# Kernel tuning notes

Hardware: AMD Instinct MI355X
Metric: run time of the kernel (lower is better)

The kernel has to match this reference:

```python
import jax, jax.numpy as jnp
import numpy as np

# --- constants matching init_kwargs / defaults in the torch module ---
N_HID = 1024
N_INP = 1
DT = 0.05
RHO = 0.99
INPUT_SCALING = 1.0
GAMMA_RANGE = (2.0, 3.0)
EPS_RANGE = (0.5, 1.5)
THETA = 0.1        # spike threshold (default arg of cell)
TAU_MEM = 20.0     # LI filter time constant (default arg of forward_li_features)
FADING = False


def setup_inputs() -> dict:
    key = jax.random.key(0)
    B, T = 128, 500
    x = jax.random.normal(key, (B, T, N_INP), dtype=jnp.float32)

    rng = np.random.default_rng(0)
    # h2h = 2*(2*rand-1), then spectral_norm_scaling to spectral radius rho
    h2h = 2.0 * (2.0 * rng.random((N_HID, N_HID)) - 1.0)
    cur_rho = np.max(np.abs(np.linalg.eigvals(h2h)))
    h2h = (h2h * (RHO / cur_rho)).astype(np.float32)
    x2h = (rng.random((N_INP, N_HID)) * INPUT_SCALING).astype(np.float32)
    bias = ((rng.random(N_HID) * 2.0 - 1.0) * INPUT_SCALING).astype(np.float32)
    gamma = (rng.random(N_HID) * (GAMMA_RANGE[1] - GAMMA_RANGE[0]) + GAMMA_RANGE[0]).astype(np.float32)
    epsilon = (rng.random(N_HID) * (EPS_RANGE[1] - EPS_RANGE[0]) + EPS_RANGE[0]).astype(np.float32)

    return {
        "x": x,
        "h2h": jnp.asarray(h2h),
        "x2h": jnp.asarray(x2h),
        "bias": jnp.asarray(bias),
        "gamma": jnp.asarray(gamma),
        "epsilon": jnp.asarray(epsilon),
    }


def reference(x, h2h, x2h, bias, gamma, epsilon):
    B, T, _ = x.shape
    n_hid = h2h.shape[0]
    dt = jnp.float32(DT)
    alpha = jnp.exp(jnp.float32(-1.0 / TAU_MEM))

    def step(carry, xt):
        hy, hz, u, tot = carry
        # coupled-oscillator cell (ref_period stays identically zero in the source)
        pre = jnp.tanh(xt @ x2h + hy @ h2h + bias)       # (B, n_hid)
        hz = hz + dt * (pre - gamma * hy - epsilon * hz)
        if FADING:
            hz = hz - dt * hz
        hy = hy + dt * hz
        if FADING:
            hy = hy - dt * hy
        s = (hy - THETA > 0).astype(jnp.float32)          # spike
        u = u * alpha + s * (1.0 - alpha)                 # LI filter
        tot = tot + s.sum()
        return (hy, hz, u, tot), None

    z = jnp.zeros((B, n_hid), dtype=jnp.float32)
    init = (z, z, z, jnp.float32(0.0))
    xs = jnp.swapaxes(x, 0, 1)                            # (T, B, n_inp)
    (hy, hz, u, tot), _ = jax.lax.scan(step, init, xs)
    avg_firing_rate = tot / (B * T * n_hid)
    return u, avg_firing_rate
```

## Files before the change

kernel.cpp:

```cpp
#include <hip/hip_runtime.h>
#include <math.h>

#define N_HID   1024
#define NBATCH  128
#define TSTEPS  500
#define DT      0.05f
#define THETA   0.1f

#define B_WG   8
#define C_WG   64
#define KSPL   8
#define KSEG   (N_HID / KSPL)
#define NGRP   (NBATCH / B_WG)
#define NCT    (N_HID / C_WG)
#define NWG    (NGRP * NCT)

typedef unsigned long long u64;


__global__ __launch_bounds__(256, 1) void persist_kernel(
    const float* __restrict__ x,
    const float* __restrict__ W,
    const float* __restrict__ x2h,
    const float* __restrict__ bias,
    const float* __restrict__ gam,
    const float* __restrict__ eps,
    float* __restrict__ hyT0,
    float* __restrict__ hyT1,
    float* __restrict__ uout,
    unsigned int* __restrict__ tot,
    unsigned int* __restrict__ bar,
    float alpha, float oma)
{
    __shared__ float sh_hyT[N_HID * B_WG];
    __shared__ float sh_part[KSPL * B_WG * C_WG];
    __shared__ float sh_out[C_WG * (B_WG + 1)];
    __shared__ unsigned int sh_cnt;

    const int tid = threadIdx.x;
    if (tid == 0) sh_cnt = 0u;

    const int bid   = blockIdx.x;
    const int xcd   = bid & 7;
    const int idx   = bid >> 3;
    const int ctile = xcd * 2 + (idx & 1);
    const int btile = idx >> 1;
    const int c0g   = ctile * C_WG;
    const int b0    = btile * B_WG;

    const int cg  = tid & 15;
    const int bg  = (tid >> 4) & 1;
    const int ks  = tid >> 5;
    const int bl0 = bg * 4;
    const int k0  = ks * KSEG;
    const float* Wp = W + (size_t)k0 * N_HID + c0g + cg * 4;

    const int bl_a = tid >> 6;
    const int bl_b = 4 + bl_a;
    const int c_e  = tid & 63;
    const int cgl  = c0g + c_e;
    const float x2h_c  = x2h[cgl];
    const float bias_c = bias[cgl];
    const float gam_c  = gam[cgl];
    const float eps_c  = eps[cgl];
    const float* xrow_a = x + (size_t)(b0 + bl_a) * TSTEPS;
    const float* xrow_b = x + (size_t)(b0 + bl_b) * TSTEPS;

    float hz_a = 0.f, hz_b = 0.f, u_a = 0.f, u_b = 0.f;
    unsigned int spikes = 0;

    unsigned int* mybar = bar + (btile << 6);

    const float* bufs[2] = { hyT0, hyT1 };

    for (int t = 0; t < TSTEPS; ++t) {
        const float* src = bufs[t & 1];
        float*       dst = (float*)bufs[(t + 1) & 1];

        {
            u64 tmp[16];
            #pragma unroll
            for (int it = 0; it < 16; ++it) {
                const int i    = it * 256 + tid;
                const int k    = i >> 2;
                const int pair = i & 3;
                const u64* sp = (const u64*)(src + (size_t)k * NBATCH + b0) + pair;
                tmp[it] = __hip_atomic_load(sp, __ATOMIC_RELAXED,
                                            __HIP_MEMORY_SCOPE_AGENT);
            }
            u64* s64 = (u64*)sh_hyT;
            #pragma unroll
            for (int it = 0; it < 16; ++it)
                s64[it * 256 + tid] = tmp[it];
        }
        __syncthreads();

        float acc[4][4];
        #pragma unroll
        for (int i = 0; i < 4; ++i)
            #pragma unroll
            for (int j = 0; j < 4; ++j) acc[i][j] = 0.f;

        #pragma unroll 8
        for (int kk = 0; kk < KSEG; ++kk) {
            const float4 hv = *(const float4*)(&sh_hyT[(k0 + kk) * B_WG + bl0]);
            const float4 wv = *(const float4*)(Wp + (size_t)kk * N_HID);
            acc[0][0] = fmaf(hv.x, wv.x, acc[0][0]);
            acc[0][1] = fmaf(hv.x, wv.y, acc[0][1]);
            acc[0][2] = fmaf(hv.x, wv.z, acc[0][2]);
            acc[0][3] = fmaf(hv.x, wv.w, acc[0][3]);
            acc[1][0] = fmaf(hv.y, wv.x, acc[1][0]);
            acc[1][1] = fmaf(hv.y, wv.y, acc[1][1]);
            acc[1][2] = fmaf(hv.y, wv.z, acc[1][2]);
            acc[1][3] = fmaf(hv.y, wv.w, acc[1][3]);
            acc[2][0] = fmaf(hv.z, wv.x, acc[2][0]);
            acc[2][1] = fmaf(hv.z, wv.y, acc[2][1]);
            acc[2][2] = fmaf(hv.z, wv.z, acc[2][2]);
            acc[2][3] = fmaf(hv.z, wv.w, acc[2][3]);
            acc[3][0] = fmaf(hv.w, wv.x, acc[3][0]);
            acc[3][1] = fmaf(hv.w, wv.y, acc[3][1]);
            acc[3][2] = fmaf(hv.w, wv.z, acc[3][2]);
            acc[3][3] = fmaf(hv.w, wv.w, acc[3][3]);
        }

        #pragma unroll
        for (int bi = 0; bi < 4; ++bi) {
            float4 v = make_float4(acc[bi][0], acc[bi][1], acc[bi][2], acc[bi][3]);
            *(float4*)(&sh_part[((ks * B_WG) + bl0 + bi) * C_WG + cg * 4]) = v;
        }
        __syncthreads();

        {
            float sum = sh_part[(0 * B_WG + bl_a) * C_WG + c_e];
            #pragma unroll
            for (int s2 = 1; s2 < KSPL; ++s2)
                sum += sh_part[(s2 * B_WG + bl_a) * C_WG + c_e];
            const float xb  = xrow_a[t];
            const float pre = tanhf(fmaf(xb, x2h_c, sum) + bias_c);
            const float hyv = sh_hyT[cgl * B_WG + bl_a];
            hz_a = fmaf(DT, pre - gam_c * hyv - eps_c * hz_a, hz_a);
            const float hyn = fmaf(DT, hz_a, hyv);
            const int s = ((hyn - THETA) > 0.f) ? 1 : 0;
            u_a = fmaf(u_a, alpha, (float)s * oma);
            spikes += (unsigned)s;
            sh_out[c_e * (B_WG + 1) + bl_a] = hyn;
        }
        {
            float sum = sh_part[(0 * B_WG + bl_b) * C_WG + c_e];
            #pragma unroll
            for (int s2 = 1; s2 < KSPL; ++s2)
                sum += sh_part[(s2 * B_WG + bl_b) * C_WG + c_e];
            const float xb  = xrow_b[t];
            const float pre = tanhf(fmaf(xb, x2h_c, sum) + bias_c);
            const float hyv = sh_hyT[cgl * B_WG + bl_b];
            hz_b = fmaf(DT, pre - gam_c * hyv - eps_c * hz_b, hz_b);
            const float hyn = fmaf(DT, hz_b, hyv);
            const int s = ((hyn - THETA) > 0.f) ? 1 : 0;
            u_b = fmaf(u_b, alpha, (float)s * oma);
            spikes += (unsigned)s;
            sh_out[c_e * (B_WG + 1) + bl_b] = hyn;
        }
        __syncthreads();

        {
            const int c2 = tid >> 2;
            const int b2 = (tid & 3) * 2;
            u64 v;
            float2 f2 = make_float2(sh_out[c2 * (B_WG + 1) + b2],
                                    sh_out[c2 * (B_WG + 1) + b2 + 1]);
            __builtin_memcpy(&v, &f2, 8);
            u64* dp = (u64*)(dst + (size_t)(c0g + c2) * NBATCH + b0 + b2);
            __hip_atomic_store(dp, v, __ATOMIC_RELAXED,
                               __HIP_MEMORY_SCOPE_AGENT);
        }
        __syncthreads();

        if (tid == 0) {
            __hip_atomic_fetch_add(mybar, 1u, __ATOMIC_RELAXED,
                                   __HIP_MEMORY_SCOPE_AGENT);
            const unsigned int target = 16u * (unsigned int)(t + 1);
            while (__hip_atomic_load(mybar, __ATOMIC_RELAXED,
                                     __HIP_MEMORY_SCOPE_AGENT) < target) {
                __builtin_amdgcn_s_sleep(1);
            }
        }
        __syncthreads();
    }

    uout[(size_t)(b0 + bl_a) * N_HID + cgl] = u_a;
    uout[(size_t)(b0 + bl_b) * N_HID + cgl] = u_b;

    unsigned int s = spikes;
    s += __shfl_down(s, 32);
    s += __shfl_down(s, 16);
    s += __shfl_down(s, 8);
    s += __shfl_down(s, 4);
    s += __shfl_down(s, 2);
    s += __shfl_down(s, 1);
    if ((tid & 63) == 0) atomicAdd(&sh_cnt, s);
    __syncthreads();
    if (tid == 0) atomicAdd(tot, sh_cnt);
}

__global__ void init_kernel(float* hyT0, unsigned int* tot, unsigned int* bar)
{
    const int i = blockIdx.x * blockDim.x + threadIdx.x;
    const int n = NBATCH * N_HID;
    if (i < n) hyT0[i] = 0.f;
    if (i == 0) *tot = 0u;
    if (i < NGRP * 64) bar[i] = 0u;
}

__global__ void final_kernel(const unsigned int* __restrict__ tot,
                             float* __restrict__ out_rate)
{
    if (threadIdx.x == 0 && blockIdx.x == 0) {
        const double denom = (double)NBATCH * (double)TSTEPS * (double)N_HID;
        *out_rate = (float)((double)(*tot) / denom);
    }
}

extern "C" void kernel_launch(void* const* d_in, const int* in_sizes, int n_in,
                              void* d_out, int out_size, void* d_ws, size_t ws_size,
                              hipStream_t stream)
{
    const float* x    = (const float*)d_in[0];
    const float* h2h  = (const float*)d_in[1];
    const float* x2h  = (const float*)d_in[2];
    const float* bias = (const float*)d_in[3];
    const float* gam  = (const float*)d_in[4];
    const float* eps  = (const float*)d_in[5];

    float* out = (float*)d_out;

    float* hyT0 = (float*)d_ws;
    float* hyT1 = hyT0 + (size_t)NBATCH * N_HID;
    unsigned int* tot = (unsigned int*)(hyT1 + (size_t)NBATCH * N_HID);
    unsigned int* bar = tot + 64;

    init_kernel<<<dim3((NBATCH * N_HID + 255) / 256), dim3(256), 0, stream>>>(
        hyT0, tot, bar);

    float alpha = expf(-1.0f / 20.0f);
    float oma   = 1.0f - alpha;

    void* args[] = {
        (void*)&x, (void*)&h2h, (void*)&x2h, (void*)&bias, (void*)&gam,
        (void*)&eps, (void*)&hyT0, (void*)&hyT1, (void*)&out, (void*)&tot,
        (void*)&bar, (void*)&alpha, (void*)&oma
    };
    hipLaunchCooperativeKernel((const void*)persist_kernel,
                               dim3(NWG), dim3(256), args, 0, stream);

    final_kernel<<<dim3(1), dim3(64), 0, stream>>>(tot, out + (size_t)NBATCH * N_HID);
}
```

Measured before the change: 3.762 ms.

## Replace group counter barrier with per-tile step flags polled per wave

The shared atomic-counter barrier, where every workgroup increments and spins, is replaced by per-column-tile step flags. Each wave polls only the four flags for the producer tiles whose hidden-state slice it loads, then loads that slice straight into its own shared region. This removes the block-wide sync after the load and one after the barrier, so waves can start their partial GEMV as soon as their inputs are ready. The first step now zero-fills shared memory instead of reading a zeroed global buffer. The gain depends on relaxed-ordering flags correctly publishing data, and one leftover no-op loop remains.

```diff
diff --git a/kernel.cpp b/kernel.cpp
--- a/kernel.cpp
+++ b/kernel.cpp
@@ -1,5 +1,8 @@
 #include <hip/hip_runtime.h>
 #include <math.h>
+
+typedef unsigned long long u64;
+typedef unsigned int u32;
 
 #define N_HID   1024
 #define NBATCH  128
@@ -15,8 +18,22 @@
 #define NCT    (N_HID / C_WG)
 #define NWG    (NGRP * NCT)
 
-typedef unsigned long long u64;
-
+#define CTRL_TOT    0
+#define CTRL_GRP    64
+#define CTRL_WORDS  (CTRL_GRP + NGRP * 64)
+
+__device__ __forceinline__ u32 a_ld32(const u32* p) {
+    return __hip_atomic_load(p, __ATOMIC_RELAXED, __HIP_MEMORY_SCOPE_AGENT);
+}
+__device__ __forceinline__ void a_st32(u32* p, u32 v) {
+    __hip_atomic_store(p, v, __ATOMIC_RELAXED, __HIP_MEMORY_SCOPE_AGENT);
+}
+__device__ __forceinline__ u64 a_ld64(const u64* p) {
+    return __hip_atomic_load(p, __ATOMIC_RELAXED, __HIP_MEMORY_SCOPE_AGENT);
+}
+__device__ __forceinline__ void a_st64(u64* p, u64 v) {
+    __hip_atomic_store(p, v, __ATOMIC_RELAXED, __HIP_MEMORY_SCOPE_AGENT);
+}
 
 __global__ __launch_bounds__(256, 1) void persist_kernel(
     const float* __restrict__ x,
@@ -28,14 +45,13 @@
     float* __restrict__ hyT0,
     float* __restrict__ hyT1,
     float* __restrict__ uout,
-    unsigned int* __restrict__ tot,
-    unsigned int* __restrict__ bar,
+    u32* __restrict__ ctrl,
     float alpha, float oma)
 {
     __shared__ float sh_hyT[N_HID * B_WG];
     __shared__ float sh_part[KSPL * B_WG * C_WG];
     __shared__ float sh_out[C_WG * (B_WG + 1)];
-    __shared__ unsigned int sh_cnt;
+    __shared__ u32 sh_cnt;
 
     const int tid = threadIdx.x;
     if (tid == 0) sh_cnt = 0u;
@@ -54,6 +70,11 @@
     const int bl0 = bg * 4;
     const int k0  = ks * KSEG;
     const float* Wp = W + (size_t)k0 * N_HID + c0g + cg * 4;
+
+    const int wv   = tid >> 6;
+    const int lane = tid & 63;
+    u32* flags = ctrl + CTRL_GRP + (btile << 6);
+    u32* myflag_pollp = flags + (4 * wv + (lane & 3));
 
     const int bl_a = tid >> 6;
     const int bl_b = 4 + bl_a;
@@ -67,60 +88,61 @@
     const float* xrow_b = x + (size_t)(b0 + bl_b) * TSTEPS;
 
     float hz_a = 0.f, hz_b = 0.f, u_a = 0.f, u_b = 0.f;
-    unsigned int spikes = 0;
-
-    unsigned int* mybar = bar + (btile << 6);
-
-    const float* bufs[2] = { hyT0, hyT1 };
+    u32 spikes = 0;
+
+    const float* src = hyT0;
+    float*       dst = hyT1;
 
     for (int t = 0; t < TSTEPS; ++t) {
-        const float* src = bufs[t & 1];
-        float*       dst = (float*)bufs[(t + 1) & 1];
-
-        {
+        if (t == 0) {
+            u64* s64 = (u64*)sh_hyT;
+            #pragma unroll
+            for (int it = 0; it < 16; ++it) s64[it * 256 + tid] = 0ull;
+            __syncthreads();
+        } else {
+            while (!__all(a_ld32(myflag_pollp) >= (u32)t))
+                __builtin_amdgcn_s_sleep(1);
             u64 tmp[16];
             #pragma unroll
             for (int it = 0; it < 16; ++it) {
-                const int i    = it * 256 + tid;
-                const int k    = i >> 2;
+                const int i    = it * 64 + lane;
+                const int k    = (wv << 8) + (i >> 2);
                 const int pair = i & 3;
                 const u64* sp = (const u64*)(src + (size_t)k * NBATCH + b0) + pair;
-                tmp[it] = __hip_atomic_load(sp, __ATOMIC_RELAXED,
-                                            __HIP_MEMORY_SCOPE_AGENT);
+                tmp[it] = a_ld64(sp);
             }
             u64* s64 = (u64*)sh_hyT;
             #pragma unroll
             for (int it = 0; it < 16; ++it)
-                s64[it * 256 + tid] = tmp[it];
-        }
-        __syncthreads();
+                s64[(wv << 10) + it * 64 + lane] = tmp[it];
+        }
 
         float acc[4][4];
         #pragma unroll
         for (int i = 0; i < 4; ++i)
             #pragma unroll
-            for (int j = 0; j < 4; ++j) acc[i][j] = 0.f;
+            for (int jj = 0; jj < 4; ++jj) acc[i][jj] = 0.f;
 
         #pragma unroll 8
         for (int kk = 0; kk < KSEG; ++kk) {
             const float4 hv = *(const float4*)(&sh_hyT[(k0 + kk) * B_WG + bl0]);
-            const float4 wv = *(const float4*)(Wp + (size_t)kk * N_HID);
-            acc[0][0] = fmaf(hv.x, wv.x, acc[0][0]);
-            acc[0][1] = fmaf(hv.x, wv.y, acc[0][1]);
-            acc[0][2] = fmaf(hv.x, wv.z, acc[0][2]);
-            acc[0][3] = fmaf(hv.x, wv.w, acc[0][3]);
-            acc[1][0] = fmaf(hv.y, wv.x, acc[1][0]);
-            acc[1][1] = fmaf(hv.y, wv.y, acc[1][1]);
-            acc[1][2] = fmaf(hv.y, wv.z, acc[1][2]);
-            acc[1][3] = fmaf(hv.y, wv.w, acc[1][3]);
-            acc[2][0] = fmaf(hv.z, wv.x, acc[2][0]);
-            acc[2][1] = fmaf(hv.z, wv.y, acc[2][1]);
-            acc[2][2] = fmaf(hv.z, wv.z, acc[2][2]);
-            acc[2][3] = fmaf(hv.z, wv.w, acc[2][3]);
-            acc[3][0] = fmaf(hv.w, wv.x, acc[3][0]);
-            acc[3][1] = fmaf(hv.w, wv.y, acc[3][1]);
-            acc[3][2] = fmaf(hv.w, wv.z, acc[3][2]);
-            acc[3][3] = fmaf(hv.w, wv.w, acc[3][3]);
+            const float4 wv4 = *(const float4*)(Wp + (size_t)kk * N_HID);
+            acc[0][0] = fmaf(hv.x, wv4.x, acc[0][0]);
+            acc[0][1] = fmaf(hv.x, wv4.y, acc[0][1]);
+            acc[0][2] = fmaf(hv.x, wv4.z, acc[0][2]);
+            acc[0][3] = fmaf(hv.x, wv4.w, acc[0][3]);
+            acc[1][0] = fmaf(hv.y, wv4.x, acc[1][0]);
+            acc[1][1] = fmaf(hv.y, wv4.y, acc[1][1]);
+            acc[1][2] = fmaf(hv.y, wv4.z, acc[1][2]);
+            acc[1][3] = fmaf(hv.y, wv4.w, acc[1][3]);
+            acc[2][0] = fmaf(hv.z, wv4.x, acc[2][0]);
+            acc[2][1] = fmaf(hv.z, wv4.y, acc[2][1]);
+            acc[2][2] = fmaf(hv.z, wv4.z, acc[2][2]);
+            acc[2][3] = fmaf(hv.z, wv4.w, acc[2][3]);
+            acc[3][0] = fmaf(hv.w, wv4.x, acc[3][0]);
+            acc[3][1] = fmaf(hv.w, wv4.y, acc[3][1]);
+            acc[3][2] = fmaf(hv.w, wv4.z, acc[3][2]);
+            acc[3][3] = fmaf(hv.w, wv4.w, acc[3][3]);
         }
 
         #pragma unroll
@@ -142,7 +164,7 @@
             const float hyn = fmaf(DT, hz_a, hyv);
             const int s = ((hyn - THETA) > 0.f) ? 1 : 0;
             u_a = fmaf(u_a, alpha, (float)s * oma);
-            spikes += (unsigned)s;
+            spikes += (u32)s;
             sh_out[c_e * (B_WG + 1) + bl_a] = hyn;
         }
         {
@@ -157,40 +179,40 @@
             const float hyn = fmaf(DT, hz_b, hyv);
             const int s = ((hyn - THETA) > 0.f) ? 1 : 0;
             u_b = fmaf(u_b, alpha, (float)s * oma);
-            spikes += (unsigned)s;
+            spikes += (u32)s;
             sh_out[c_e * (B_WG + 1) + bl_b] = hyn;
         }
         __syncthreads();
 
+        {
+            const int c2 = tid >> 3;
+            #pragma unroll
+            for (int rr = 0; rr < 2; ++rr) {
+                const int c3 = c2 + rr * 32;
+                const int b2 = (tid & 7);
+                (void)c3; (void)b2;
+            }
+        }
         {
             const int c2 = tid >> 2;
             const int b2 = (tid & 3) * 2;
-            u64 v;
             float2 f2 = make_float2(sh_out[c2 * (B_WG + 1) + b2],
                                     sh_out[c2 * (B_WG + 1) + b2 + 1]);
+            u64 v;
             __builtin_memcpy(&v, &f2, 8);
-            u64* dp = (u64*)(dst + (size_t)(c0g + c2) * NBATCH + b0 + b2);
-            __hip_atomic_store(dp, v, __ATOMIC_RELAXED,
-                               __HIP_MEMORY_SCOPE_AGENT);
+            a_st64((u64*)(dst + (size_t)(c0g + c2) * NBATCH + b0 + b2), v);
         }
         __syncthreads();
 
-        if (tid == 0) {
-            __hip_atomic_fetch_add(mybar, 1u, __ATOMIC_RELAXED,
-                                   __HIP_MEMORY_SCOPE_AGENT);
-            const unsigned int target = 16u * (unsigned int)(t + 1);
-            while (__hip_atomic_load(mybar, __ATOMIC_RELAXED,
-                                     __HIP_MEMORY_SCOPE_AGENT) < target) {
-                __builtin_amdgcn_s_sleep(1);
-            }
-        }
-        __syncthreads();
+        if (tid == 0) a_st32(flags + ctile, (u32)(t + 1));
+
+        float* tmpp = (float*)src; src = dst; dst = tmpp;
     }
 
     uout[(size_t)(b0 + bl_a) * N_HID + cgl] = u_a;
     uout[(size_t)(b0 + bl_b) * N_HID + cgl] = u_b;
 
-    unsigned int s = spikes;
+    u32 s = spikes;
     s += __shfl_down(s, 32);
     s += __shfl_down(s, 16);
     s += __shfl_down(s, 8);
@@ -199,24 +221,24 @@
     s += __shfl_down(s, 1);
     if ((tid & 63) == 0) atomicAdd(&sh_cnt, s);
     __syncthreads();
-    if (tid == 0) atomicAdd(tot, sh_cnt);
-}
-
-__global__ void init_kernel(float* hyT0, unsigned int* tot, unsigned int* bar)
+    if (tid == 0) atomicAdd(ctrl + CTRL_TOT, sh_cnt);
+}
+
+__global__ void init_kernel(u32* ctrl)
 {
     const int i = blockIdx.x * blockDim.x + threadIdx.x;
-    const int n = NBATCH * N_HID;
-    if (i < n) hyT0[i] = 0.f;
-    if (i == 0) *tot = 0u;
-    if (i < NGRP * 64) bar[i] = 0u;
-}
-
-__global__ void final_kernel(const unsigned int* __restrict__ tot,
+    if (i < CTRL_WORDS) {
+        __hip_atomic_store(ctrl + i, 0u, __ATOMIC_RELAXED,
+                           __HIP_MEMORY_SCOPE_AGENT);
+    }
+}
+
+__global__ void final_kernel(const u32* __restrict__ ctrl,
                              float* __restrict__ out_rate)
 {
     if (threadIdx.x == 0 && blockIdx.x == 0) {
         const double denom = (double)NBATCH * (double)TSTEPS * (double)N_HID;
-        *out_rate = (float)((double)(*tot) / denom);
+        *out_rate = (float)((double)ctrl[CTRL_TOT] / denom);
     }
 }
 
@@ -235,22 +257,21 @@
 
     float* hyT0 = (float*)d_ws;
     float* hyT1 = hyT0 + (size_t)NBATCH * N_HID;
-    unsigned int* tot = (unsigned int*)(hyT1 + (size_t)NBATCH * N_HID);
-    unsigned int* bar = tot + 64;
-
-    init_kernel<<<dim3((NBATCH * N_HID + 255) / 256), dim3(256), 0, stream>>>(
-        hyT0, tot, bar);
+    u32*   ctrl = (u32*)(hyT1 + (size_t)NBATCH * N_HID);
+
+    init_kernel<<<dim3((CTRL_WORDS + 255) / 256), dim3(256), 0, stream>>>(ctrl);
 
     float alpha = expf(-1.0f / 20.0f);
     float oma   = 1.0f - alpha;
 
     void* args[] = {
         (void*)&x, (void*)&h2h, (void*)&x2h, (void*)&bias, (void*)&gam,
-        (void*)&eps, (void*)&hyT0, (void*)&hyT1, (void*)&out, (void*)&tot,
-        (void*)&bar, (void*)&alpha, (void*)&oma
+        (void*)&eps, (void*)&hyT0, (void*)&hyT1, (void*)&out, (void*)&ctrl,
+        (void*)&alpha, (void*)&oma
     };
     hipLaunchCooperativeKernel((const void*)persist_kernel,
                                dim3(NWG), dim3(256), args, 0, stream);
 
-    final_kernel<<<dim3(1), dim3(64), 0, stream>>>(tot, out + (size_t)NBATCH * N_HID);
-}
+    final_kernel<<<dim3(1), dim3(64), 0, stream>>>(
+        ctrl, out + (size_t)NBATCH * N_HID);
+}
```

After: 3.665 ms. 1.03x faster.
